# Kernel optimization log

Measured on AMD Instinct MI355X. Metric: run time of the kernel, lower is better.

## Reference

```python
import jax, jax.numpy as jnp
import numpy as np

D_MODEL = 1024
D_FF = 4096
BATCH = 4
SEQ = 4096
DILATION = 1


def _dw_causal_conv(x, w, dilation):
    # x: [B, S, D], w: [D, 1, K] (depthwise, torch Conv1d groups=D layout)
    k = w.shape[-1]
    pad = (k - 1) * dilation
    h = jnp.transpose(x, (0, 2, 1))  # [B, D, S]
    out = jax.lax.conv_general_dilated(
        h, w,
        window_strides=(1,),
        padding=[(pad, 0)],  # causal left pad
        rhs_dilation=(dilation,),
        dimension_numbers=('NCH', 'OIH', 'NCH'),
        feature_group_count=h.shape[1],
    )
    return jnp.transpose(out, (0, 2, 1))  # [B, S, D]


def _rmsnorm(x, w):
    ms = jnp.mean(jnp.square(x), axis=-1, keepdims=True)
    return x * jax.lax.rsqrt(ms + 1e-6) * w


def setup_inputs() -> dict:
    key = jax.random.key(0)
    ks = jax.random.split(key, 12)
    s = lambda d: 1.0 / np.sqrt(d)
    return {
        'x': jax.random.normal(ks[0], (BATCH, SEQ, D_MODEL), jnp.float32),
        'ln1_w': jnp.ones((D_MODEL,), jnp.float32),
        'ln2_w': jnp.ones((D_MODEL,), jnp.float32),
        'w_fine': jax.random.normal(ks[1], (D_MODEL, 1, 3), jnp.float32) * 0.5,
        'w_medium': jax.random.normal(ks[2], (D_MODEL, 1, 5), jnp.float32) * 0.4,
        'w_coarse': jax.random.normal(ks[3], (D_MODEL, 1, 7), jnp.float32) * 0.3,
        'sg_w': jax.random.normal(ks[4], (3, D_MODEL), jnp.float32) * 0.02,
        'up_w': jax.random.normal(ks[5], (2 * D_MODEL, D_MODEL), jnp.float32) * s(D_MODEL),
        'down_w': jax.random.normal(ks[6], (D_MODEL, D_MODEL), jnp.float32) * s(D_MODEL),
        'wg': jax.random.normal(ks[7], (D_FF, D_MODEL), jnp.float32) * s(D_MODEL),
        'wu': jax.random.normal(ks[8], (D_FF, D_MODEL), jnp.float32) * s(D_MODEL),
        'wo': jax.random.normal(ks[9], (D_MODEL, D_FF), jnp.float32) * s(D_FF),
    }


def reference(x, ln1_w, ln2_w, w_fine, w_medium, w_coarse, sg_w, up_w, down_w, wg, wu, wo):
    # --- MSAC mixer with pre-norm residual ---
    h = _rmsnorm(x, ln1_w)
    gv = jnp.einsum('bsd,ed->bse', h, up_w)        # [B, S, 2D]
    gate, val = jnp.split(gv, 2, axis=-1)
    gate = jax.nn.sigmoid(gate)
    c_fine = _dw_causal_conv(val, w_fine, DILATION)
    c_medium = _dw_causal_conv(val, w_medium, DILATION)
    c_coarse = _dw_causal_conv(val, w_coarse, DILATION)
    scale_w = jax.nn.softmax(jnp.einsum('bsd,ed->bse', h, sg_w), axis=-1)  # [B, S, 3]
    fused = (scale_w[..., 0:1] * c_fine
             + scale_w[..., 1:2] * c_medium
             + scale_w[..., 2:3] * c_coarse)
    x = x + jnp.einsum('bsd,ed->bse', fused * gate, down_w)
    # --- SwiGLU FFN with pre-norm residual ---
    h2 = _rmsnorm(x, ln2_w)
    g = jax.nn.silu(jnp.einsum('bsd,fd->bsf', h2, wg))
    u = jnp.einsum('bsd,fd->bsf', h2, wu)
    x = x + jnp.einsum('bsf,df->bsd', g * u, wo)
    return x
```

## Files before the change

kernel.cpp:

```cpp
#include <hip/hip_runtime.h>
#include <stdint.h>

#define D_MODEL 1024
#define D_FF    4096
#define NTOK    16384
#define SEQ     4096

typedef __bf16 bf16x8 __attribute__((ext_vector_type(8)));
typedef float  f32x4  __attribute__((ext_vector_type(4)));

typedef __attribute__((address_space(1))) void gvoid;
typedef __attribute__((address_space(3))) void svoid;

__device__ __forceinline__ unsigned short f2bf(float f) {
  union { float f; uint32_t u; } v; v.f = f;
  uint32_t u = v.u;
  u += 0x7FFFu + ((u >> 16) & 1u);
  return (unsigned short)(u >> 16);
}
__device__ __forceinline__ float bf2f(unsigned short h) {
  union { uint32_t u; float f; } v; v.u = ((uint32_t)h) << 16;
  return v.f;
}

__device__ __forceinline__ void gload16(const void* g, void* l) {
  __builtin_amdgcn_global_load_lds((gvoid*)g, (svoid*)l, 16, 0, 0);
}

__device__ __forceinline__ float fast_sigmoid(float x) {
  return __builtin_amdgcn_rcpf(1.f + __expf(-x));
}

__global__ __launch_bounds__(256) void cvt_all_k(
    const float* __restrict__ up, const float* __restrict__ dn,
    const float* __restrict__ wo, const float* __restrict__ wg,
    const float* __restrict__ wu,
    unsigned short* __restrict__ d_up, unsigned short* __restrict__ d_dn,
    unsigned short* __restrict__ d_wo, unsigned short* __restrict__ d_il)
{
  const int i = blockIdx.x * 256 + threadIdx.x;
  const float* src;
  unsigned short* dst;
  if (i < 524288) {
    src = up + (size_t)i * 4;            dst = d_up + (size_t)i * 4;
  } else if (i < 786432) {
    const int j = i - 524288;
    src = dn + (size_t)j * 4;            dst = d_dn + (size_t)j * 4;
  } else if (i < 1835008) {
    const int j = i - 786432;
    src = wo + (size_t)j * 4;            dst = d_wo + (size_t)j * 4;
  } else {
    const int j = i - 1835008;
    const int row = j >> 8, c4 = j & 255;
    const int gi = row >> 5, w = row & 31;
    src = (w < 16 ? wg + (size_t)(gi * 16 + w) * 1024
                  : wu + (size_t)(gi * 16 + (w - 16)) * 1024) + c4 * 4;
    dst = d_il + (size_t)j * 4;
  }
  float4 f = *reinterpret_cast<const float4*>(src);
  ushort4 o;
  o.x = f2bf(f.x); o.y = f2bf(f.y); o.z = f2bf(f.z); o.w = f2bf(f.w);
  *reinterpret_cast<ushort4*>(dst) = o;
}

template<bool SG>
__global__ __launch_bounds__(256) void rmsnorm_k(
    const float* __restrict__ X, const float* __restrict__ W,
    const float* __restrict__ SGW,
    unsigned short* __restrict__ H, float* __restrict__ SCL)
{
  const int n = blockIdx.x;
  const int t = threadIdx.x;
  float4 x = reinterpret_cast<const float4*>(X + (size_t)n * D_MODEL)[t];
  float4 w = reinterpret_cast<const float4*>(W)[t];
  float4 hw;
  hw.x = x.x * w.x; hw.y = x.y * w.y; hw.z = x.z * w.z; hw.w = x.w * w.w;
  float ss = x.x*x.x + x.y*x.y + x.z*x.z + x.w*x.w;
  float p0 = 0.f, p1 = 0.f, p2 = 0.f;
  if (SG) {
    float4 s0 = reinterpret_cast<const float4*>(SGW)[t];
    float4 s1 = reinterpret_cast<const float4*>(SGW + D_MODEL)[t];
    float4 s2 = reinterpret_cast<const float4*>(SGW + 2 * D_MODEL)[t];
    p0 = hw.x*s0.x + hw.y*s0.y + hw.z*s0.z + hw.w*s0.w;
    p1 = hw.x*s1.x + hw.y*s1.y + hw.z*s1.z + hw.w*s1.w;
    p2 = hw.x*s2.x + hw.y*s2.y + hw.z*s2.z + hw.w*s2.w;
  }
  #pragma unroll
  for (int off = 32; off > 0; off >>= 1) {
    ss += __shfl_xor(ss, off);
    if (SG) {
      p0 += __shfl_xor(p0, off);
      p1 += __shfl_xor(p1, off);
      p2 += __shfl_xor(p2, off);
    }
  }
  __shared__ float red[4][4];
  const int wid = t >> 6;
  if ((t & 63) == 0) { red[wid][0] = ss; red[wid][1] = p0; red[wid][2] = p1; red[wid][3] = p2; }
  __syncthreads();
  ss = red[0][0] + red[1][0] + red[2][0] + red[3][0];
  const float r = rsqrtf(ss * (1.0f / D_MODEL) + 1e-6f);
  ushort4 h4;
  h4.x = f2bf(hw.x * r); h4.y = f2bf(hw.y * r); h4.z = f2bf(hw.z * r); h4.w = f2bf(hw.w * r);
  reinterpret_cast<ushort4*>(H + (size_t)n * D_MODEL)[t] = h4;
  if (SG && t == 0) {
    float l0 = (red[0][1] + red[1][1] + red[2][1] + red[3][1]) * r;
    float l1 = (red[0][2] + red[1][2] + red[2][2] + red[3][2]) * r;
    float l2 = (red[0][3] + red[1][3] + red[2][3] + red[3][3]) * r;
    float mx = fmaxf(l0, fmaxf(l1, l2));
    float e0 = expf(l0 - mx), e1 = expf(l1 - mx), e2 = expf(l2 - mx);
    float inv = 1.f / (e0 + e1 + e2);
    SCL[n * 3 + 0] = e0 * inv; SCL[n * 3 + 1] = e1 * inv; SCL[n * 3 + 2] = e2 * inv;
  }
}

__global__ __launch_bounds__(256) void conv_k(
    const unsigned short* __restrict__ GV,
    const float* __restrict__ SCL,
    const float* __restrict__ W3, const float* __restrict__ W5, const float* __restrict__ W7,
    unsigned short* __restrict__ Y)
{
  const int n = blockIdx.x;
  const int t = threadIdx.x;
  const int d0 = t * 4;
  const int s = n & (SEQ - 1);
  const unsigned short* vbase = GV + (size_t)n * (2 * D_MODEL) + D_MODEL + d0;
  float v[7][4];
  #pragma unroll
  for (int j = 0; j < 7; ++j) {
    const int tap = 6 - j;
    if (tap <= s) {
      ushort4 u = *reinterpret_cast<const ushort4*>(vbase - (size_t)tap * (2 * D_MODEL));
      v[j][0] = bf2f(u.x); v[j][1] = bf2f(u.y); v[j][2] = bf2f(u.z); v[j][3] = bf2f(u.w);
    } else {
      v[j][0] = 0.f; v[j][1] = 0.f; v[j][2] = 0.f; v[j][3] = 0.f;
    }
  }
  ushort4 gb = *reinterpret_cast<const ushort4*>(GV + (size_t)n * (2 * D_MODEL) + d0);
  float gf[4] = { bf2f(gb.x), bf2f(gb.y), bf2f(gb.z), bf2f(gb.w) };
  const float sc0 = SCL[n * 3 + 0], sc1 = SCL[n * 3 + 1], sc2 = SCL[n * 3 + 2];
  ushort4 out;
  unsigned short o[4];
  #pragma unroll
  for (int i = 0; i < 4; ++i) {
    const int d = d0 + i;
    float c3 = W3[d*3+0]*v[4][i] + W3[d*3+1]*v[5][i] + W3[d*3+2]*v[6][i];
    float c5 = W5[d*5+0]*v[2][i] + W5[d*5+1]*v[3][i] + W5[d*5+2]*v[4][i]
             + W5[d*5+3]*v[5][i] + W5[d*5+4]*v[6][i];
    float c7 = 0.f;
    #pragma unroll
    for (int j = 0; j < 7; ++j) c7 += W7[d*7+j] * v[j][i];
    const float g = fast_sigmoid(gf[i]);
    o[i] = f2bf((sc0 * c3 + sc1 * c5 + sc2 * c7) * g);
  }
  out.x = o[0]; out.y = o[1]; out.z = o[2]; out.w = o[3];
  reinterpret_cast<ushort4*>(Y + (size_t)n * D_MODEL)[t] = out;
}


#define EPI_BF16      0
#define EPI_RES       1
#define EPI_SWIGLU_IL 2

#define STAGE_A(tt, h) do { \
    char* d_ = dstBase + (((tt)&1) << 16) + ((h) << 14); \
    const unsigned short* s_ = aSrc + (size_t)((h)*128) * K + (tt)*64; \
    gload16(s_, d_); gload16(s_ + (size_t)64 * K, d_ + 8192); } while(0)

#define STAGE_B(tt, h) do { \
    char* d_ = dstBase + (((tt)&1) << 16) + 32768 + ((h) << 14); \
    const unsigned short* s_ = bSrc + (size_t)((h)*32) * K + (tt)*64; \
    gload16(s_, d_); gload16(s_ + (size_t)128 * K, d_ + 8192); } while(0)

#define DSR(dst, base, IMM) \
  asm volatile("ds_read_b128 %0, %1 offset:" #IMM : "=v"(dst) : "v"(base))

#define RD_B0(S) do { \
  DSR(b0[0][0], bB##S##k0, 0);    DSR(b0[0][1], bB##S##k1, 0); \
  DSR(b0[1][0], bB##S##k0, 2048); DSR(b0[1][1], bB##S##k1, 2048); } while(0)

#define RD_B1(S) do { \
  DSR(b1[0][0], bB##S##k0, 16384); DSR(b1[0][1], bB##S##k1, 16384); \
  DSR(b1[1][0], bB##S##k0, 18432); DSR(b1[1][1], bB##S##k1, 18432); } while(0)

#define RD_AQ0A(S) do { \
  DSR(aq[0][0], aA##S##k0, 0);    DSR(aq[0][1], aA##S##k1, 0); \
  DSR(aq[1][0], aA##S##k0, 2048); DSR(aq[1][1], aA##S##k1, 2048); } while(0)

#define RD_AQ0B(S) do { \
  DSR(aq[2][0], aA##S##k0, 4096); DSR(aq[2][1], aA##S##k1, 4096); \
  DSR(aq[3][0], aA##S##k0, 6144); DSR(aq[3][1], aA##S##k1, 6144); } while(0)

#define RD_AQ1A(S) do { \
  DSR(aq[0][0], aA##S##k0, 8192);  DSR(aq[0][1], aA##S##k1, 8192); \
  DSR(aq[1][0], aA##S##k0, 10240); DSR(aq[1][1], aA##S##k1, 10240); } while(0)

#define RD_AQ1B(S) do { \
  DSR(aq[2][0], aA##S##k0, 12288); DSR(aq[2][1], aA##S##k1, 12288); \
  DSR(aq[3][0], aA##S##k0, 14336); DSR(aq[3][1], aA##S##k1, 14336); } while(0)

#define MMAQ(BR, MQ, NQ) do { \
  _Pragma("unroll") for (int f_ = 0; f_ < 4; ++f_) \
  _Pragma("unroll") for (int e_ = 0; e_ < 2; ++e_) { \
    acc[(MQ)*4+f_][(NQ)*2+e_] = __builtin_amdgcn_mfma_f32_16x16x32_bf16( \
        aq[f_][0], BR[e_][0], acc[(MQ)*4+f_][(NQ)*2+e_], 0, 0, 0); \
    acc[(MQ)*4+f_][(NQ)*2+e_] = __builtin_amdgcn_mfma_f32_16x16x32_bf16( \
        aq[f_][1], BR[e_][1], acc[(MQ)*4+f_][(NQ)*2+e_], 0, 0, 0); \
  } } while(0)

#define MMAQH(BR, MQ, NQ, F0) do { \
  _Pragma("unroll") for (int f_ = (F0); f_ < (F0) + 2; ++f_) \
  _Pragma("unroll") for (int e_ = 0; e_ < 2; ++e_) { \
    acc[(MQ)*4+f_][(NQ)*2+e_] = __builtin_amdgcn_mfma_f32_16x16x32_bf16( \
        aq[f_][0], BR[e_][0], acc[(MQ)*4+f_][(NQ)*2+e_], 0, 0, 0); \
    acc[(MQ)*4+f_][(NQ)*2+e_] = __builtin_amdgcn_mfma_f32_16x16x32_bf16( \
        aq[f_][1], BR[e_][1], acc[(MQ)*4+f_][(NQ)*2+e_], 0, 0, 0); \
  } } while(0)

#define GATE8 do { asm volatile("s_waitcnt lgkmcnt(8)" ::: "memory"); \
                   __builtin_amdgcn_sched_barrier(0); } while(0)
#define GATE4 do { asm volatile("s_waitcnt lgkmcnt(4)" ::: "memory"); \
                   __builtin_amdgcn_sched_barrier(0); } while(0)
#define GATE0 do { asm volatile("s_waitcnt lgkmcnt(0)" ::: "memory"); \
                   __builtin_amdgcn_sched_barrier(0); } while(0)
#define VM4   asm volatile("s_waitcnt vmcnt(4)" ::: "memory")
#define VM0   asm volatile("s_waitcnt vmcnt(0)" ::: "memory")
#define BAR   __builtin_amdgcn_s_barrier()
#define PRIO1 __builtin_amdgcn_s_setprio(1)
#define PRIO0 __builtin_amdgcn_s_setprio(0)

#define PHASE_ROW0(S) do { \
  RD_B0(S); RD_AQ0A(S); RD_AQ0B(S); RD_B1(S); \
  GATE8; PRIO1; MMAQH(b0, 0, 0, 0); PRIO0; \
  GATE4; PRIO1; MMAQH(b0, 0, 0, 2); PRIO0; \
  GATE0; PRIO1; MMAQ(b1, 0, 1); PRIO0; \
} while(0)

#define PHASE_ROW1(S) do { \
  RD_AQ1A(S); RD_AQ1B(S); \
  GATE4; PRIO1; MMAQH(b1, 1, 1, 0); MMAQH(b0, 1, 0, 0); PRIO0; \
  GATE0; PRIO1; MMAQH(b1, 1, 1, 2); MMAQH(b0, 1, 0, 2); PRIO0; \
} while(0)

template<int EPI>
__global__ __launch_bounds__(512, 2) void gemm256_k(
    const unsigned short* __restrict__ A,
    const unsigned short* __restrict__ B0g,
    const float* __restrict__ RES,
    void* __restrict__ OUT,
    int M, int N, int K)
{
  __shared__ uint4 lds4[8192];
  char* lbase = (char*)lds4;

  const int tid  = threadIdx.x;
  const int lane = tid & 63;
  const int wid  = tid >> 6;
  const int wm   = wid >> 2;
  const int wn   = wid & 3;
  const int l15 = lane & 15, l4 = lane >> 4, l7 = lane & 7;
  const int m0 = blockIdx.x * 256;
  const int n0 = blockIdx.y * 256;
  const int nt = K >> 6;

  const int r0 = tid >> 3;
  const int kc = (tid & 7) ^ (r0 & 7);
  const unsigned short* aSrc = A + (size_t)(m0 + r0) * K + kc * 8;
  const unsigned short* bSrc = B0g + (size_t)(n0 + (r0 >> 5) * 64 + (r0 & 31)) * K + kc * 8;
  char* dstBase = lbase + tid * 16;

  const unsigned colswz = (unsigned)((l4 ^ l7) << 4);
  const unsigned aA0k0 = (unsigned)((wm << 14) + l15 * 128) + colswz;
  const unsigned aA0k1 = aA0k0 ^ 0x40u;
  const unsigned aA1k0 = aA0k0 + 65536u;
  const unsigned aA1k1 = aA0k1 + 65536u;
  const unsigned bB0k0 = (unsigned)(32768 + (wn * 32 + l15) * 128) + colswz;
  const unsigned bB0k1 = bB0k0 ^ 0x40u;
  const unsigned bB1k0 = bB0k0 + 65536u;
  const unsigned bB1k1 = bB0k1 + 65536u;

  f32x4 acc[8][4];
  #pragma unroll
  for (int i = 0; i < 8; ++i)
    #pragma unroll
    for (int j = 0; j < 4; ++j)
      #pragma unroll
      for (int r = 0; r < 4; ++r) acc[i][j][r] = 0.f;

  bf16x8 aq[4][2], b0[2][2], b1[2][2];

  STAGE_A(0, 0); STAGE_A(0, 1); STAGE_B(0, 0); STAGE_B(0, 1);
  STAGE_B(1, 0); STAGE_B(1, 1);
  VM4;
  BAR;

  for (int t = 0; t + 2 < nt; t += 2) {
    STAGE_A(t + 1, 0); STAGE_A(t + 1, 1);
    PHASE_ROW0(0);
    BAR;
    STAGE_B(t + 2, 0); STAGE_B(t + 2, 1);
    PHASE_ROW1(0);
    VM4;
    BAR;
    STAGE_A(t + 2, 0); STAGE_A(t + 2, 1);
    PHASE_ROW0(1);
    BAR;
    STAGE_B(t + 3, 0); STAGE_B(t + 3, 1);
    PHASE_ROW1(1);
    VM4;
    BAR;
  }

  {
    STAGE_A(nt - 1, 0); STAGE_A(nt - 1, 1);
    PHASE_ROW0(0);
    BAR;
    PHASE_ROW1(0);
    VM0;
    BAR;
    PHASE_ROW0(1);
    BAR;
    PHASE_ROW1(1);
    BAR;
  }

  if (M < -1) ((float*)OUT)[tid] = ((float*)lds4)[tid];

  const int cr = (lane >> 4) * 4;
  const int cc = lane & 15;
  if (EPI == EPI_SWIGLU_IL) {
    const int ffbase = (n0 + wn * 64) >> 1;
    #pragma unroll
    for (int F = 0; F < 8; ++F)
      #pragma unroll
      for (int p = 0; p < 2; ++p)
        #pragma unroll
        for (int rr = 0; rr < 4; ++rr) {
          const int grow = m0 + wm * 128 + (F >> 2) * 64 + (F & 3) * 16 + cr + rr;
          const float g = acc[F][2 * p][rr];
          const float u = acc[F][2 * p + 1][rr];
          const float o = g * fast_sigmoid(g) * u;
          ((unsigned short*)OUT)[(size_t)grow * D_FF + ffbase + p * 16 + cc] = f2bf(o);
        }
  } else {
    #pragma unroll
    for (int F = 0; F < 8; ++F)
      #pragma unroll
      for (int E = 0; E < 4; ++E)
        #pragma unroll
        for (int rr = 0; rr < 4; ++rr) {
          const int grow = m0 + wm * 128 + (F >> 2) * 64 + (F & 3) * 16 + cr + rr;
          const int gcol = n0 + wn * 64 + (E >> 1) * 32 + (E & 1) * 16 + cc;
          const float v = acc[F][E][rr];
          if (EPI == EPI_BF16) {
            ((unsigned short*)OUT)[(size_t)grow * N + gcol] = f2bf(v);
          } else {
            const size_t idx = (size_t)grow * N + gcol;
            ((float*)OUT)[idx] = RES[idx] + v;
          }
        }
  }
}

extern "C" void kernel_launch(void* const* d_in, const int* in_sizes, int n_in,
                              void* d_out, int out_size, void* d_ws, size_t ws_size,
                              hipStream_t stream)
{
  const float* x    = (const float*)d_in[0];
  const float* ln1w = (const float*)d_in[1];
  const float* ln2w = (const float*)d_in[2];
  const float* wf   = (const float*)d_in[3];
  const float* wm   = (const float*)d_in[4];
  const float* wco  = (const float*)d_in[5];
  const float* sgw  = (const float*)d_in[6];
  const float* upw  = (const float*)d_in[7];
  const float* dnw  = (const float*)d_in[8];
  const float* wg   = (const float*)d_in[9];
  const float* wu   = (const float*)d_in[10];
  const float* wo   = (const float*)d_in[11];

  char* ws = (char*)d_ws;
  size_t off = 0;
  auto alloc = [&](size_t bytes) -> void* {
    void* p = ws + off;
    off += (bytes + 255) & ~(size_t)255;
    return p;
  };
  unsigned short* wb_up = (unsigned short*)alloc((size_t)2048 * 1024 * 2);
  unsigned short* wb_dn = (unsigned short*)alloc((size_t)1024 * 1024 * 2);
  unsigned short* wb_il = (unsigned short*)alloc((size_t)8192 * 1024 * 2);
  unsigned short* wb_wo = (unsigned short*)alloc((size_t)1024 * 4096 * 2);
  float*          scl   = (float*)alloc((size_t)NTOK * 3 * 4);
  unsigned short* h2b   = (unsigned short*)alloc((size_t)NTOK * D_MODEL * 2);
  char* big = (char*)alloc((size_t)NTOK * 4096 * 2);
  unsigned short* hb  = (unsigned short*)big;
  unsigned short* gvb = (unsigned short*)(big + (size_t)NTOK * 1024 * 2);
  unsigned short* yb  = (unsigned short*)(big + (size_t)NTOK * 3072 * 2);
  unsigned short* gub = (unsigned short*)big;
  float* x1 = (float*)d_out;

  cvt_all_k<<<15360, 256, 0, stream>>>(upw, dnw, wo, wg, wu,
                                       wb_up, wb_dn, wb_wo, wb_il);

  rmsnorm_k<true><<<NTOK, 256, 0, stream>>>(x, ln1w, sgw, hb, scl);
  gemm256_k<EPI_BF16><<<dim3(64, 8), 512, 0, stream>>>(hb, wb_up, nullptr, gvb, NTOK, 2048, 1024);
  conv_k<<<NTOK, 256, 0, stream>>>(gvb, scl, wf, wm, wco, yb);
  gemm256_k<EPI_RES><<<dim3(64, 4), 512, 0, stream>>>(yb, wb_dn, x, x1, NTOK, 1024, 1024);
  rmsnorm_k<false><<<NTOK, 256, 0, stream>>>(x1, ln2w, nullptr, h2b, nullptr);
  gemm256_k<EPI_SWIGLU_IL><<<dim3(64, 32), 512, 0, stream>>>(h2b, wb_il, nullptr, gub, NTOK, 8192, 1024);
  gemm256_k<EPI_RES><<<dim3(64, 4), 512, 0, stream>>>(gub, wb_wo, x1, (float*)d_out, NTOK, 1024, 4096);
}
```

Measured before the change: 669.0 us.

## Add 4-wave 256x256 GEMM kernel with 128x128 per-wave tiles for SwiGLU

Adds a new GEMM kernel for the gate/up projection that uses 4 waves (256 threads) per 256x256 block, so each wave computes a 128x128 tile instead of 8 waves with 128x64 tiles. The larger per-wave tile raises operand reuse from LDS, meaning fewer ds_reads per MFMA. The trade-off is more accumulator registers and one block per CU (launch_bounds 256,1), which lowers occupancy and latency hiding. The 8-wave kernel also drops its SwiGLU epilogue and merges two A-fragment read phases.

```diff
diff --git a/kernel.cpp b/kernel.cpp
--- a/kernel.cpp
+++ b/kernel.cpp
@@ -157,10 +157,27 @@
   reinterpret_cast<ushort4*>(Y + (size_t)n * D_MODEL)[t] = out;
 }
 
-
 #define EPI_BF16      0
 #define EPI_RES       1
 #define EPI_SWIGLU_IL 2
+
+#define DSR(dst, base, IMM) \
+  asm volatile("ds_read_b128 %0, %1 offset:" #IMM : "=v"(dst) : "v"(base))
+
+#define GATE12 do { asm volatile("s_waitcnt lgkmcnt(12)" ::: "memory"); \
+                    __builtin_amdgcn_sched_barrier(0); } while(0)
+#define GATE8  do { asm volatile("s_waitcnt lgkmcnt(8)" ::: "memory"); \
+                    __builtin_amdgcn_sched_barrier(0); } while(0)
+#define GATE4  do { asm volatile("s_waitcnt lgkmcnt(4)" ::: "memory"); \
+                    __builtin_amdgcn_sched_barrier(0); } while(0)
+#define GATE0  do { asm volatile("s_waitcnt lgkmcnt(0)" ::: "memory"); \
+                    __builtin_amdgcn_sched_barrier(0); } while(0)
+#define VM4   asm volatile("s_waitcnt vmcnt(4)" ::: "memory")
+#define VM8   asm volatile("s_waitcnt vmcnt(8)" ::: "memory")
+#define VM0   asm volatile("s_waitcnt vmcnt(0)" ::: "memory")
+#define BAR   __builtin_amdgcn_s_barrier()
+#define PRIO1 __builtin_amdgcn_s_setprio(1)
+#define PRIO0 __builtin_amdgcn_s_setprio(0)
 
 #define STAGE_A(tt, h) do { \
     char* d_ = dstBase + (((tt)&1) << 16) + ((h) << 14); \
@@ -172,9 +189,6 @@
     const unsigned short* s_ = bSrc + (size_t)((h)*32) * K + (tt)*64; \
     gload16(s_, d_); gload16(s_ + (size_t)128 * K, d_ + 8192); } while(0)
 
-#define DSR(dst, base, IMM) \
-  asm volatile("ds_read_b128 %0, %1 offset:" #IMM : "=v"(dst) : "v"(base))
-
 #define RD_B0(S) do { \
   DSR(b0[0][0], bB##S##k0, 0);    DSR(b0[0][1], bB##S##k1, 0); \
   DSR(b0[1][0], bB##S##k0, 2048); DSR(b0[1][1], bB##S##k1, 2048); } while(0)
@@ -183,11 +197,9 @@
   DSR(b1[0][0], bB##S##k0, 16384); DSR(b1[0][1], bB##S##k1, 16384); \
   DSR(b1[1][0], bB##S##k0, 18432); DSR(b1[1][1], bB##S##k1, 18432); } while(0)
 
-#define RD_AQ0A(S) do { \
+#define RD_AQ0(S) do { \
   DSR(aq[0][0], aA##S##k0, 0);    DSR(aq[0][1], aA##S##k1, 0); \
-  DSR(aq[1][0], aA##S##k0, 2048); DSR(aq[1][1], aA##S##k1, 2048); } while(0)
-
-#define RD_AQ0B(S) do { \
+  DSR(aq[1][0], aA##S##k0, 2048); DSR(aq[1][1], aA##S##k1, 2048); \
   DSR(aq[2][0], aA##S##k0, 4096); DSR(aq[2][1], aA##S##k1, 4096); \
   DSR(aq[3][0], aA##S##k0, 6144); DSR(aq[3][1], aA##S##k1, 6144); } while(0)
 
@@ -217,22 +229,9 @@
         aq[f_][1], BR[e_][1], acc[(MQ)*4+f_][(NQ)*2+e_], 0, 0, 0); \
   } } while(0)
 
-#define GATE8 do { asm volatile("s_waitcnt lgkmcnt(8)" ::: "memory"); \
-                   __builtin_amdgcn_sched_barrier(0); } while(0)
-#define GATE4 do { asm volatile("s_waitcnt lgkmcnt(4)" ::: "memory"); \
-                   __builtin_amdgcn_sched_barrier(0); } while(0)
-#define GATE0 do { asm volatile("s_waitcnt lgkmcnt(0)" ::: "memory"); \
-                   __builtin_amdgcn_sched_barrier(0); } while(0)
-#define VM4   asm volatile("s_waitcnt vmcnt(4)" ::: "memory")
-#define VM0   asm volatile("s_waitcnt vmcnt(0)" ::: "memory")
-#define BAR   __builtin_amdgcn_s_barrier()
-#define PRIO1 __builtin_amdgcn_s_setprio(1)
-#define PRIO0 __builtin_amdgcn_s_setprio(0)
-
 #define PHASE_ROW0(S) do { \
-  RD_B0(S); RD_AQ0A(S); RD_AQ0B(S); RD_B1(S); \
-  GATE8; PRIO1; MMAQH(b0, 0, 0, 0); PRIO0; \
-  GATE4; PRIO1; MMAQH(b0, 0, 0, 2); PRIO0; \
+  RD_B0(S); RD_AQ0(S); RD_B1(S); \
+  GATE4; PRIO1; MMAQ(b0, 0, 0); PRIO0; \
   GATE0; PRIO1; MMAQ(b1, 0, 1); PRIO0; \
 } while(0)
 
@@ -310,7 +309,6 @@
     VM4;
     BAR;
   }
-
   {
     STAGE_A(nt - 1, 0); STAGE_A(nt - 1, 1);
     PHASE_ROW0(0);
@@ -328,38 +326,178 @@
 
   const int cr = (lane >> 4) * 4;
   const int cc = lane & 15;
-  if (EPI == EPI_SWIGLU_IL) {
-    const int ffbase = (n0 + wn * 64) >> 1;
+  #pragma unroll
+  for (int F = 0; F < 8; ++F)
     #pragma unroll
-    for (int F = 0; F < 8; ++F)
+    for (int E = 0; E < 4; ++E)
       #pragma unroll
-      for (int p = 0; p < 2; ++p)
-        #pragma unroll
-        for (int rr = 0; rr < 4; ++rr) {
-          const int grow = m0 + wm * 128 + (F >> 2) * 64 + (F & 3) * 16 + cr + rr;
-          const float g = acc[F][2 * p][rr];
-          const float u = acc[F][2 * p + 1][rr];
-          const float o = g * fast_sigmoid(g) * u;
-          ((unsigned short*)OUT)[(size_t)grow * D_FF + ffbase + p * 16 + cc] = f2bf(o);
+      for (int rr = 0; rr < 4; ++rr) {
+        const int grow = m0 + wm * 128 + (F >> 2) * 64 + (F & 3) * 16 + cr + rr;
+        const int gcol = n0 + wn * 64 + (E >> 1) * 32 + (E & 1) * 16 + cc;
+        const float v = acc[F][E][rr];
+        if (EPI == EPI_BF16) {
+          ((unsigned short*)OUT)[(size_t)grow * N + gcol] = f2bf(v);
+        } else {
+          const size_t idx = (size_t)grow * N + gcol;
+          ((float*)OUT)[idx] = RES[idx] + v;
         }
-  } else {
+      }
+}
+
+
+#define WSTAGE_A(tt, h) do { \
+    char* d_ = dstBaseW + (((tt)&1) << 16) + ((h) << 14); \
+    const unsigned short* s_ = aSrcW + (size_t)((h)*128) * K + (tt)*64; \
+    gload16(s_, d_);                     gload16(s_ + (size_t)32 * K, d_ + 4096); \
+    gload16(s_ + (size_t)64 * K, d_ + 8192); gload16(s_ + (size_t)96 * K, d_ + 12288); } while(0)
+
+#define WSTAGE_B(tt, h) do { \
+    char* d_ = dstBaseW + (((tt)&1) << 16) + 32768 + ((h) << 14); \
+    const unsigned short* s_ = bSrcW + (size_t)((h)*128) * K + (tt)*64; \
+    gload16(s_, d_);                     gload16(s_ + (size_t)32 * K, d_ + 4096); \
+    gload16(s_ + (size_t)64 * K, d_ + 8192); gload16(s_ + (size_t)96 * K, d_ + 12288); } while(0)
+
+#define WRD_A0(S) do { \
+  DSR(aq[0][0], aW##S##k0, 0);    DSR(aq[0][1], aW##S##k1, 0); \
+  DSR(aq[1][0], aW##S##k0, 2048); DSR(aq[1][1], aW##S##k1, 2048); \
+  DSR(aq[2][0], aW##S##k0, 4096); DSR(aq[2][1], aW##S##k1, 4096); \
+  DSR(aq[3][0], aW##S##k0, 6144); DSR(aq[3][1], aW##S##k1, 6144); } while(0)
+
+#define WRD_A1(S) do { \
+  DSR(aq[0][0], aW##S##k0, 8192);  DSR(aq[0][1], aW##S##k1, 8192); \
+  DSR(aq[1][0], aW##S##k0, 10240); DSR(aq[1][1], aW##S##k1, 10240); \
+  DSR(aq[2][0], aW##S##k0, 12288); DSR(aq[2][1], aW##S##k1, 12288); \
+  DSR(aq[3][0], aW##S##k0, 14336); DSR(aq[3][1], aW##S##k1, 14336); } while(0)
+
+#define WRD_B(S) do { \
+  DSR(bq[0][0], bW##S##k0, 0);     DSR(bq[0][1], bW##S##k1, 0); \
+  DSR(bq[1][0], bW##S##k0, 2048);  DSR(bq[1][1], bW##S##k1, 2048); \
+  DSR(bq[2][0], bW##S##k0, 4096);  DSR(bq[2][1], bW##S##k1, 4096); \
+  DSR(bq[3][0], bW##S##k0, 6144);  DSR(bq[3][1], bW##S##k1, 6144); \
+  DSR(bq[4][0], bW##S##k0, 8192);  DSR(bq[4][1], bW##S##k1, 8192); \
+  DSR(bq[5][0], bW##S##k0, 10240); DSR(bq[5][1], bW##S##k1, 10240); \
+  DSR(bq[6][0], bW##S##k0, 12288); DSR(bq[6][1], bW##S##k1, 12288); \
+  DSR(bq[7][0], bW##S##k0, 14336); DSR(bq[7][1], bW##S##k1, 14336); } while(0)
+
+#define WMMA(AOFF, F0, NF, E0, NE) do { \
+  _Pragma("unroll") for (int f_ = (F0); f_ < (F0) + (NF); ++f_) \
+  _Pragma("unroll") for (int e_ = (E0); e_ < (E0) + (NE); ++e_) { \
+    acc[(AOFF)+f_][e_] = __builtin_amdgcn_mfma_f32_16x16x32_bf16( \
+        aq[f_][0], bq[e_][0], acc[(AOFF)+f_][e_], 0, 0, 0); \
+    acc[(AOFF)+f_][e_] = __builtin_amdgcn_mfma_f32_16x16x32_bf16( \
+        aq[f_][1], bq[e_][1], acc[(AOFF)+f_][e_], 0, 0, 0); \
+  } } while(0)
+
+#define WPHASE0(S) do { \
+  WRD_A0(S); WRD_B(S); \
+  GATE12; PRIO1; WMMA(0, 0, 4, 0, 2); PRIO0; \
+  GATE8;  PRIO1; WMMA(0, 0, 4, 2, 2); PRIO0; \
+  GATE4;  PRIO1; WMMA(0, 0, 4, 4, 2); PRIO0; \
+  GATE0;  PRIO1; WMMA(0, 0, 4, 6, 2); PRIO0; \
+} while(0)
+
+#define WPHASE1(S) do { \
+  WRD_A1(S); \
+  GATE4; PRIO1; WMMA(4, 0, 2, 0, 8); PRIO0; \
+  GATE0; PRIO1; WMMA(4, 2, 2, 0, 8); PRIO0; \
+} while(0)
+
+__global__ __launch_bounds__(256, 1) void gemm256w4_k(
+    const unsigned short* __restrict__ A,
+    const unsigned short* __restrict__ B0g,
+    void* __restrict__ OUT,
+    int M, int N, int K)
+{
+  __shared__ uint4 lds4[8192];
+  char* lbase = (char*)lds4;
+
+  const int tid  = threadIdx.x;
+  const int lane = tid & 63;
+  const int wid  = tid >> 6;
+  const int wm   = wid >> 1;
+  const int wn   = wid & 1;
+  const int l15 = lane & 15, l4 = lane >> 4, l7 = lane & 7;
+  const int m0 = blockIdx.x * 256;
+  const int n0 = blockIdx.y * 256;
+  const int nt = K >> 6;
+
+  const int r0 = tid >> 3;
+  const int kc = (tid & 7) ^ (r0 & 7);
+  const unsigned short* aSrcW = A + (size_t)(m0 + r0) * K + kc * 8;
+  const unsigned short* bSrcW = B0g + (size_t)(n0 + r0) * K + kc * 8;
+  char* dstBaseW = lbase + tid * 16;
+
+  const unsigned colswz = (unsigned)((l4 ^ l7) << 4);
+  const unsigned aW0k0 = (unsigned)((wm << 14) + l15 * 128) + colswz;
+  const unsigned aW0k1 = aW0k0 ^ 0x40u;
+  const unsigned aW1k0 = aW0k0 + 65536u;
+  const unsigned aW1k1 = aW0k1 + 65536u;
+  const unsigned bW0k0 = (unsigned)(32768 + (wn << 14) + l15 * 128) + colswz;
+  const unsigned bW0k1 = bW0k0 ^ 0x40u;
+  const unsigned bW1k0 = bW0k0 + 65536u;
+  const unsigned bW1k1 = bW0k1 + 65536u;
+
+  f32x4 acc[8][8];
+  #pragma unroll
+  for (int i = 0; i < 8; ++i)
     #pragma unroll
-    for (int F = 0; F < 8; ++F)
+    for (int j = 0; j < 8; ++j)
       #pragma unroll
-      for (int E = 0; E < 4; ++E)
-        #pragma unroll
-        for (int rr = 0; rr < 4; ++rr) {
-          const int grow = m0 + wm * 128 + (F >> 2) * 64 + (F & 3) * 16 + cr + rr;
-          const int gcol = n0 + wn * 64 + (E >> 1) * 32 + (E & 1) * 16 + cc;
-          const float v = acc[F][E][rr];
-          if (EPI == EPI_BF16) {
-            ((unsigned short*)OUT)[(size_t)grow * N + gcol] = f2bf(v);
-          } else {
-            const size_t idx = (size_t)grow * N + gcol;
-            ((float*)OUT)[idx] = RES[idx] + v;
-          }
-        }
-  }
+      for (int r = 0; r < 4; ++r) acc[i][j][r] = 0.f;
+
+  bf16x8 aq[4][2], bq[8][2];
+
+  WSTAGE_A(0, 0); WSTAGE_A(0, 1); WSTAGE_B(0, 0); WSTAGE_B(0, 1);
+  WSTAGE_B(1, 0); WSTAGE_B(1, 1);
+  VM8;
+  BAR;
+
+  for (int t = 0; t + 2 < nt; t += 2) {
+    WSTAGE_A(t + 1, 0); WSTAGE_A(t + 1, 1);
+    WPHASE0(0);
+    BAR;
+    WSTAGE_B(t + 2, 0); WSTAGE_B(t + 2, 1);
+    WPHASE1(0);
+    VM8;
+    BAR;
+    WSTAGE_A(t + 2, 0); WSTAGE_A(t + 2, 1);
+    WPHASE0(1);
+    BAR;
+    WSTAGE_B(t + 3, 0); WSTAGE_B(t + 3, 1);
+    WPHASE1(1);
+    VM8;
+    BAR;
+  }
+  {
+    WSTAGE_A(nt - 1, 0); WSTAGE_A(nt - 1, 1);
+    WPHASE0(0);
+    BAR;
+    WPHASE1(0);
+    VM0;
+    BAR;
+    WPHASE0(1);
+    BAR;
+    WPHASE1(1);
+    BAR;
+  }
+
+  if (M < -1) ((float*)OUT)[tid] = ((float*)lds4)[tid];
+
+  const int cr = (lane >> 4) * 4;
+  const int cc = lane & 15;
+  const int ffbase = (n0 + wn * 128) >> 1;
+  #pragma unroll
+  for (int F = 0; F < 8; ++F)
+    #pragma unroll
+    for (int p = 0; p < 4; ++p)
+      #pragma unroll
+      for (int rr = 0; rr < 4; ++rr) {
+        const int grow = m0 + wm * 128 + F * 16 + cr + rr;
+        const float g = acc[F][2 * p][rr];
+        const float u = acc[F][2 * p + 1][rr];
+        const float o = g * fast_sigmoid(g) * u;
+        ((unsigned short*)OUT)[(size_t)grow * D_FF + ffbase + p * 16 + cc] = f2bf(o);
+      }
 }
 
 extern "C" void kernel_launch(void* const* d_in, const int* in_sizes, int n_in,
@@ -407,6 +545,6 @@
   conv_k<<<NTOK, 256, 0, stream>>>(gvb, scl, wf, wm, wco, yb);
   gemm256_k<EPI_RES><<<dim3(64, 4), 512, 0, stream>>>(yb, wb_dn, x, x1, NTOK, 1024, 1024);
   rmsnorm_k<false><<<NTOK, 256, 0, stream>>>(x1, ln2w, nullptr, h2b, nullptr);
-  gemm256_k<EPI_SWIGLU_IL><<<dim3(64, 32), 512, 0, stream>>>(h2b, wb_il, nullptr, gub, NTOK, 8192, 1024);
+  gemm256w4_k<<<dim3(64, 32), 256, 0, stream>>>(h2b, wb_il, gub, NTOK, 8192, 1024);
   gemm256_k<EPI_RES><<<dim3(64, 4), 512, 0, stream>>>(gub, wb_wo, x1, (float*)d_out, NTOK, 1024, 4096);
 }
```

After: 820.1 us. 1.23x slower.
